# Performance work log

Measured on AMD Instinct MI355X. Metric: run time of the kernel, lower is better.

## Reference

```python
import jax, jax.numpy as jnp
import numpy as np
import math

N_HEADS = 8

def setup_inputs() -> dict:
    key = jax.random.key(0)
    ks = jax.random.split(key, 5)
    B, S, D = 2, 4096, 512
    return {
        "x": jax.random.normal(ks[0], (B, S, D), jnp.float32),
        "W_in": jax.random.normal(ks[1], (D, 3 * D), jnp.float32) * (1.0 / math.sqrt(D)),
        "b_in": jax.random.normal(ks[2], (3 * D,), jnp.float32) * 0.02,
        "W_out": jax.random.normal(ks[3], (D, D), jnp.float32) * (1.0 / math.sqrt(D)),
        "b_out": jax.random.normal(ks[4], (D,), jnp.float32) * 0.02,
        "causal_mask": 1,
    }

def reference(x, W_in, b_in, W_out, b_out, causal_mask):
    B, S, D = x.shape
    H = N_HEADS
    dh = D // H
    qkv = x @ W_in + b_in                      # [B,S,3D]
    q, k, v = jnp.split(qkv, 3, axis=-1)
    # [B,S,D] -> [B,H,S,dh]
    q = q.reshape(B, S, H, dh).transpose(0, 2, 1, 3)
    k = k.reshape(B, S, H, dh).transpose(0, 2, 1, 3)
    v = v.reshape(B, S, H, dh).transpose(0, 2, 1, 3)
    scores = jnp.einsum("bhqd,bhkd->bhqk", q, k)  # [B,H,S,S]
    if causal_mask:
        # strictly upper triangle masked to -inf (before scaling, as in torch code)
        causal = jnp.tril(jnp.ones((S, S), dtype=bool))
        scores = jnp.where(causal, scores, -jnp.inf)
    scores = scores / math.sqrt(dh)
    w = jax.nn.softmax(scores, axis=-1)
    out = jnp.einsum("bhqk,bhkd->bhqd", w, v)     # [B,H,S,dh]
    out = out.transpose(0, 2, 1, 3).reshape(B, S, D)
    return out @ W_out + b_out
```

## Files before the change

kernel.cpp:

```cpp
#include <hip/hip_runtime.h>
#include <stdint.h>

typedef __attribute__((ext_vector_type(8))) short bf16x8;
typedef __attribute__((ext_vector_type(4))) float f32x4;

__device__ __forceinline__ float bf2f(unsigned short b) {
  union { unsigned int u; float f; } c; c.u = ((unsigned int)b) << 16; return c.f;
}
__device__ __forceinline__ unsigned short f2bf(float f) {
  union { float f; unsigned int u; } c; c.f = f;
  unsigned int u = c.u;
  return (unsigned short)((u + 0x7fffu + ((u >> 16) & 1u)) >> 16);
}

__device__ __forceinline__ void gload_lds16(const void* g, void* l) {
  __builtin_amdgcn_global_load_lds((const __attribute__((address_space(1))) void*)g,
                                   (__attribute__((address_space(3))) void*)l,
                                   16, 0, 0);
}

#define QSCALE 0.18033688011112042f


__global__ __launch_bounds__(256) void cvt_x(const float* __restrict__ in,
                                             unsigned short* __restrict__ out, int n4) {
  int i = blockIdx.x * 256 + threadIdx.x;
  if (i < n4) {
    float4 f = ((const float4*)in)[i];
    ushort4 o;
    o.x = f2bf(f.x); o.y = f2bf(f.y); o.z = f2bf(f.z); o.w = f2bf(f.w);
    ((ushort4*)out)[i] = o;
  }
}

__global__ __launch_bounds__(256)
void tw_cvt_t(const float* __restrict__ W, unsigned short* __restrict__ Wt, int N) {
  __shared__ unsigned short T[64][68];
  const int n0 = blockIdx.x * 64, k0 = blockIdx.y * 64;
  const int c = threadIdx.x & 15, r = threadIdx.x >> 4;
#pragma unroll
  for (int i = 0; i < 4; ++i) {
    float4 f = *(const float4*)&W[(size_t)(k0 + i * 16 + r) * N + n0 + c * 4];
    T[c * 4 + 0][i * 16 + r] = f2bf(f.x);
    T[c * 4 + 1][i * 16 + r] = f2bf(f.y);
    T[c * 4 + 2][i * 16 + r] = f2bf(f.z);
    T[c * 4 + 3][i * 16 + r] = f2bf(f.w);
  }
  __syncthreads();
#pragma unroll
  for (int i = 0; i < 4; ++i)
    *(ushort4*)&Wt[(size_t)(n0 + i * 16 + r) * 512 + k0 + c * 4] =
        *(const ushort4*)&T[i * 16 + r][c * 4];
}

__global__ __launch_bounds__(256)
void vtr(const unsigned short* __restrict__ vsd, unsigned short* __restrict__ vt) {
  __shared__ unsigned short T[64][68];
  const int bh = blockIdx.y, s0 = blockIdx.x * 64;
  const int c = threadIdx.x & 15, r = threadIdx.x >> 4;
#pragma unroll
  for (int i = 0; i < 4; ++i) {
    ushort4 u = *(const ushort4*)&vsd[((size_t)bh * 4096 + s0 + i * 16 + r) * 64 + c * 4];
    T[c * 4 + 0][i * 16 + r] = u.x;
    T[c * 4 + 1][i * 16 + r] = u.y;
    T[c * 4 + 2][i * 16 + r] = u.z;
    T[c * 4 + 3][i * 16 + r] = u.w;
  }
  __syncthreads();
#pragma unroll
  for (int i = 0; i < 4; ++i)
    *(ushort4*)&vt[((size_t)bh * 64 + i * 16 + r) * 4096 + s0 + c * 4] =
        *(const ushort4*)&T[i * 16 + r][c * 4];
}


template<int QKV>
__global__ __launch_bounds__(256)
void gemm_bt(const unsigned short* __restrict__ A, const unsigned short* __restrict__ Bt,
             const float* __restrict__ bias, float* __restrict__ Cout,
             unsigned short* __restrict__ qo, unsigned short* __restrict__ ko,
             unsigned short* __restrict__ vo, int M, int N, int K) {
  __shared__ unsigned short As[128 * 64];
  __shared__ unsigned short Bs[128 * 64];
  const int tid = threadIdx.x;
  const int wid = tid >> 6;
  const int lane = tid & 63;
  const int row0 = blockIdx.x * 128;
  const int col0 = blockIdx.y * 128;

  f32x4 acc[4][4];
#pragma unroll
  for (int m = 0; m < 4; ++m)
#pragma unroll
    for (int n = 0; n < 4; ++n)
      acc[m][n] = (f32x4){0.f, 0.f, 0.f, 0.f};

  const int wr = (wid >> 1) * 64;
  const int wc = (wid & 1) * 64;
  const int rw = lane & 15;
  const int nk = K >> 6;

  for (int kt = 0; kt < nk; ++kt) {
    const int k0 = kt << 6;
#pragma unroll
    for (int i = 0; i < 4; ++i) {
      int c = i * 256 + tid;
      int r = c >> 3, kq = (c & 7) << 3;
      gload_lds16(A + (size_t)(row0 + r) * K + k0 + kq, As + (size_t)(i * 256 + wid * 64) * 8);
    }
#pragma unroll
    for (int i = 0; i < 4; ++i) {
      int c = i * 256 + tid;
      int r = c >> 3, kq = (c & 7) << 3;
      gload_lds16(Bt + (size_t)(col0 + r) * K + k0 + kq, Bs + (size_t)(i * 256 + wid * 64) * 8);
    }
    __syncthreads();
#pragma unroll
    for (int ks = 0; ks < 2; ++ks) {
      const int kof = ks * 32 + (lane >> 4) * 8;
      bf16x8 af[4], bfr[4];
#pragma unroll
      for (int m = 0; m < 4; ++m)
        af[m] = *(const bf16x8*)&As[(wr + m * 16 + rw) * 64 + kof];
#pragma unroll
      for (int n = 0; n < 4; ++n)
        bfr[n] = *(const bf16x8*)&Bs[(wc + n * 16 + rw) * 64 + kof];
#pragma unroll
      for (int m = 0; m < 4; ++m)
#pragma unroll
        for (int n = 0; n < 4; ++n)
          acc[m][n] = __builtin_amdgcn_mfma_f32_16x16x32_bf16(af[m], bfr[n], acc[m][n], 0, 0, 0);
    }
    __syncthreads();
  }

  const int lr4 = (lane >> 4) * 4;
  const int lc = lane & 15;
#pragma unroll
  for (int m = 0; m < 4; ++m) {
#pragma unroll
    for (int n = 0; n < 4; ++n) {
      const int col = col0 + wc + n * 16 + lc;
      const float bb = bias[col];
      const int row = row0 + wr + m * 16 + lr4;
      if (QKV) {
        const int which = col >> 9;
        const int rem = col & 511, h = rem >> 6, d = rem & 63;
        const int b = row >> 12, s = row & 4095;
        const float scale = (which == 0) ? QSCALE : 1.0f;
        unsigned short* dst = (which == 0) ? qo : ((which == 1) ? ko : vo);
#pragma unroll
        for (int r2 = 0; r2 < 4; ++r2)
          dst[(((size_t)(b * 8 + h) * 4096 + (s + r2)) << 6) + d] =
              f2bf((acc[m][n][r2] + bb) * scale);
      } else {
#pragma unroll
        for (int r2 = 0; r2 < 4; ++r2)
          Cout[(size_t)(row + r2) * N + col] = acc[m][n][r2] + bb;
      }
    }
  }
}


__global__ __launch_bounds__(256, 3)
void attn_mfma(const unsigned short* __restrict__ Qb, const unsigned short* __restrict__ Kb,
               const unsigned short* __restrict__ Vtb, unsigned short* __restrict__ Ob,
               const int* __restrict__ causal_p) {
  __shared__ unsigned short Ks[2][64 * 64];
  __shared__ unsigned short Vs[2][64 * 64];
  __shared__ unsigned short Ps[4][32 * 64];

  const int tid = threadIdx.x;
  const int wid = tid >> 6;
  const int lane = tid & 63;
  const int lx = lane & 15, ly = lane >> 4, l7 = lane & 7;
  const int p = 31 - blockIdx.x;
  const int bh = blockIdx.y;
  const int causal = *causal_p;
  const int qw = p * 128 + wid * 32;
  const size_t qkbase = (size_t)bh * 4096 * 64;
  const size_t vbase = (size_t)bh * 64 * 4096;

  bf16x8 qf[2][2];
#pragma unroll
  for (int rf = 0; rf < 2; ++rf)
#pragma unroll
    for (int ks = 0; ks < 2; ++ks)
      qf[rf][ks] =
          *(const bf16x8*)(Qb + qkbase + (size_t)(qw + rf * 16 + lx) * 64 + ks * 32 + ly * 8);

  f32x4 o[2][4];
  float mrow[2][4], lpart[2][4];
#pragma unroll
  for (int rf = 0; rf < 2; ++rf) {
#pragma unroll
    for (int df = 0; df < 4; ++df) o[rf][df] = (f32x4){0.f, 0.f, 0.f, 0.f};
#pragma unroll
    for (int r = 0; r < 4; ++r) { mrow[rf][r] = -1e30f; lpart[rf][r] = 0.f; }
  }

  const int ktmax = causal ? (2 * p + 1) : 63;

#pragma unroll
  for (int pass = 0; pass < 2; ++pass) {
    int c = pass * 256 + tid;
    int r = c >> 3, ch = c & 7;
    gload_lds16(Kb + qkbase + (size_t)r * 64 + ((ch ^ (r & 7)) << 3),
                &Ks[0][(size_t)(pass * 256 + wid * 64) * 8]);
    gload_lds16(Vtb + vbase + (size_t)r * 4096 + ((ch ^ (r & 7)) << 3),
                &Vs[0][(size_t)(pass * 256 + wid * 64) * 8]);
  }
  __syncthreads();

  int cur = 0;
  for (int kt = 0; kt <= ktmax; ++kt) {
    if (kt < ktmax) {
      const int nx = kt + 1;
#pragma unroll
      for (int pass = 0; pass < 2; ++pass) {
        int c = pass * 256 + tid;
        int r = c >> 3, ch = c & 7;
        gload_lds16(Kb + qkbase + (size_t)(nx * 64 + r) * 64 + ((ch ^ (r & 7)) << 3),
                    &Ks[cur ^ 1][(size_t)(pass * 256 + wid * 64) * 8]);
        gload_lds16(Vtb + vbase + (size_t)r * 4096 + nx * 64 + ((ch ^ (r & 7)) << 3),
                    &Vs[cur ^ 1][(size_t)(pass * 256 + wid * 64) * 8]);
      }
    }

    const int ktb = kt * 64;
    if (!causal || ktb <= qw + 31) {
      f32x4 s[2][4];
#pragma unroll
      for (int rf = 0; rf < 2; ++rf)
#pragma unroll
        for (int cf = 0; cf < 4; ++cf) s[rf][cf] = (f32x4){0.f, 0.f, 0.f, 0.f};
#pragma unroll
      for (int ks = 0; ks < 2; ++ks) {
        const int kel = ((ks * 4 + ly) ^ l7) << 3;
        bf16x8 kf[4];
#pragma unroll
        for (int cf = 0; cf < 4; ++cf)
          kf[cf] = *(const bf16x8*)&Ks[cur][(cf * 16 + lx) * 64 + kel];
#pragma unroll
        for (int rf = 0; rf < 2; ++rf)
#pragma unroll
          for (int cf = 0; cf < 4; ++cf)
            s[rf][cf] = __builtin_amdgcn_mfma_f32_16x16x32_bf16(qf[rf][ks], kf[cf], s[rf][cf], 0, 0, 0);
      }

      const bool diag = causal && (ktb + 63 > qw);
      float tmx[2][4];
      bool ok = true;
#pragma unroll
      for (int rf = 0; rf < 2; ++rf) {
#pragma unroll
        for (int r = 0; r < 4; ++r) {
          if (diag) {
            const int qg = qw + rf * 16 + ly * 4 + r;
#pragma unroll
            for (int cf = 0; cf < 4; ++cf)
              if (ktb + cf * 16 + lx > qg) s[rf][cf][r] = -1e30f;
          }
          const float a0 = fmaxf(s[rf][0][r], s[rf][1][r]);
          const float a1 = fmaxf(s[rf][2][r], s[rf][3][r]);
          tmx[rf][r] = fmaxf(a0, a1);
          ok = ok && (tmx[rf][r] <= mrow[rf][r] + 8.f);
        }
      }

      if (__all(ok)) {
#pragma unroll
        for (int rf = 0; rf < 2; ++rf) {
#pragma unroll
          for (int r = 0; r < 4; ++r) {
            const float mo = mrow[rf][r];
            const int ql = rf * 16 + ly * 4 + r;
            const int swz = (ql & 7) << 3;
            float lp = 0.f;
#pragma unroll
            for (int cf = 0; cf < 4; ++cf) {
              const float pv = __builtin_amdgcn_exp2f(s[rf][cf][r] - mo);
              lp += pv;
              Ps[wid][ql * 64 + ((cf * 16 + lx) ^ swz)] = f2bf(pv);
            }
            lpart[rf][r] += lp;
          }
        }
      } else {
#pragma unroll
        for (int rf = 0; rf < 2; ++rf) {
#pragma unroll
          for (int r = 0; r < 4; ++r) {
            float tm = tmx[rf][r];
            tm = fmaxf(tm, __shfl_xor(tm, 1));
            tm = fmaxf(tm, __shfl_xor(tm, 2));
            tm = fmaxf(tm, __shfl_xor(tm, 4));
            tm = fmaxf(tm, __shfl_xor(tm, 8));
            const float mo = mrow[rf][r];
            const float mn = fmaxf(mo, tm);
            const float scl = __builtin_amdgcn_exp2f(mo - mn);
            const int ql = rf * 16 + ly * 4 + r;
            const int swz = (ql & 7) << 3;
            float lp = 0.f;
#pragma unroll
            for (int cf = 0; cf < 4; ++cf) {
              const float pv = __builtin_amdgcn_exp2f(s[rf][cf][r] - mn);
              lp += pv;
              Ps[wid][ql * 64 + ((cf * 16 + lx) ^ swz)] = f2bf(pv);
            }
            lpart[rf][r] = lpart[rf][r] * scl + lp;
            mrow[rf][r] = mn;
#pragma unroll
            for (int df = 0; df < 4; ++df) o[rf][df][r] *= scl;
          }
        }
      }

#pragma unroll
      for (int ks = 0; ks < 2; ++ks) {
        const int kel = ((ks * 4 + ly) ^ l7) << 3;
        bf16x8 pa[2], vf[4];
#pragma unroll
        for (int rf = 0; rf < 2; ++rf)
          pa[rf] = *(const bf16x8*)&Ps[wid][(rf * 16 + lx) * 64 + kel];
#pragma unroll
        for (int df = 0; df < 4; ++df)
          vf[df] = *(const bf16x8*)&Vs[cur][(df * 16 + lx) * 64 + kel];
#pragma unroll
        for (int rf = 0; rf < 2; ++rf)
#pragma unroll
          for (int df = 0; df < 4; ++df)
            o[rf][df] = __builtin_amdgcn_mfma_f32_16x16x32_bf16(pa[rf], vf[df], o[rf][df], 0, 0, 0);
      }
    }
    __syncthreads();
    cur ^= 1;
  }

  const int b = bh >> 3, h = bh & 7;
#pragma unroll
  for (int rf = 0; rf < 2; ++rf) {
#pragma unroll
    for (int r = 0; r < 4; ++r) {
      float l = lpart[rf][r];
      l += __shfl_xor(l, 1);
      l += __shfl_xor(l, 2);
      l += __shfl_xor(l, 4);
      l += __shfl_xor(l, 8);
      const float inv = 1.0f / l;
      const int row = b * 4096 + qw + rf * 16 + ly * 4 + r;
#pragma unroll
      for (int df = 0; df < 4; ++df)
        Ob[(size_t)row * 512 + h * 64 + df * 16 + lx] = f2bf(o[rf][df][r] * inv);
    }
  }
}


extern "C" void kernel_launch(void* const* d_in, const int* in_sizes, int n_in,
                              void* d_out, int out_size, void* d_ws, size_t ws_size,
                              hipStream_t stream) {
  const float* x     = (const float*)d_in[0];
  const float* W_in  = (const float*)d_in[1];
  const float* b_in  = (const float*)d_in[2];
  const float* W_out = (const float*)d_in[3];
  const float* b_out = (const float*)d_in[4];
  const int* causal  = (const int*)d_in[5];
  float* out = (float*)d_out;

  unsigned short* xb   = (unsigned short*)d_ws;
  unsigned short* wint = xb + 4194304;
  unsigned short* wout = wint + 786432;
  unsigned short* qb   = wout + 262144;
  unsigned short* kb   = qb + 4194304;
  unsigned short* vt   = kb + 4194304;
  unsigned short* vsd  = (unsigned short*)d_out;

  cvt_x<<<4096, 256, 0, stream>>>(x, xb, 1048576);
  tw_cvt_t<<<dim3(24, 8), 256, 0, stream>>>(W_in, wint, 1536);
  tw_cvt_t<<<dim3(8, 8), 256, 0, stream>>>(W_out, wout, 512);

  gemm_bt<1><<<dim3(64, 12), 256, 0, stream>>>(xb, wint, b_in, nullptr, qb, kb, vsd,
                                               8192, 1536, 512);

  vtr<<<dim3(64, 16), 256, 0, stream>>>(vsd, vt);

  attn_mfma<<<dim3(32, 16), 256, 0, stream>>>(qb, kb, vt, xb, causal);

  gemm_bt<0><<<dim3(64, 4), 256, 0, stream>>>(xb, wout, b_out, out, nullptr, nullptr, nullptr,
                                              8192, 512, 512);
}
```

Measured before the change: 385.2 us.

## Use single-wave attention blocks reading K/V directly from global memory

The attention kernel goes from 4-wave blocks, which shared double-buffered K/V tiles in LDS, to one-wave blocks covering 32 query rows each. Each wave now loads K and V fragments straight from global memory, with no LDS staging and no block barriers. The grid is reordered so that heads vary fastest and the longest causal rows are scheduled first. This removes the syncs and LDS traffic, but K/V reuse across waves is lost, so global/L2 traffic roughly quadruples and there is no prefetch to hide load latency.

```diff
diff --git a/kernel.cpp b/kernel.cpp
--- a/kernel.cpp
+++ b/kernel.cpp
@@ -163,22 +163,18 @@
 }
 
 
-__global__ __launch_bounds__(256, 3)
+__global__ __launch_bounds__(64, 3)
 void attn_mfma(const unsigned short* __restrict__ Qb, const unsigned short* __restrict__ Kb,
                const unsigned short* __restrict__ Vtb, unsigned short* __restrict__ Ob,
                const int* __restrict__ causal_p) {
-  __shared__ unsigned short Ks[2][64 * 64];
-  __shared__ unsigned short Vs[2][64 * 64];
-  __shared__ unsigned short Ps[4][32 * 64];
-
-  const int tid = threadIdx.x;
-  const int wid = tid >> 6;
-  const int lane = tid & 63;
+  __shared__ unsigned short Ps[32 * 64];
+
+  const int lane = threadIdx.x;
   const int lx = lane & 15, ly = lane >> 4, l7 = lane & 7;
-  const int p = 31 - blockIdx.x;
-  const int bh = blockIdx.y;
+  const int bh = blockIdx.x;
+  const int p = 127 - (int)blockIdx.y;
+  const int qw = p * 32;
   const int causal = *causal_p;
-  const int qw = p * 128 + wid * 32;
   const size_t qkbase = (size_t)bh * 4096 * 64;
   const size_t vbase = (size_t)bh * 64 * 4096;
 
@@ -200,142 +196,115 @@
     for (int r = 0; r < 4; ++r) { mrow[rf][r] = -1e30f; lpart[rf][r] = 0.f; }
   }
 
-  const int ktmax = causal ? (2 * p + 1) : 63;
-
-#pragma unroll
-  for (int pass = 0; pass < 2; ++pass) {
-    int c = pass * 256 + tid;
-    int r = c >> 3, ch = c & 7;
-    gload_lds16(Kb + qkbase + (size_t)r * 64 + ((ch ^ (r & 7)) << 3),
-                &Ks[0][(size_t)(pass * 256 + wid * 64) * 8]);
-    gload_lds16(Vtb + vbase + (size_t)r * 4096 + ((ch ^ (r & 7)) << 3),
-                &Vs[0][(size_t)(pass * 256 + wid * 64) * 8]);
-  }
-  __syncthreads();
-
-  int cur = 0;
+  const int ktmax = causal ? ((p * 32 + 31) >> 6) : 63;
+
   for (int kt = 0; kt <= ktmax; ++kt) {
-    if (kt < ktmax) {
-      const int nx = kt + 1;
-#pragma unroll
-      for (int pass = 0; pass < 2; ++pass) {
-        int c = pass * 256 + tid;
-        int r = c >> 3, ch = c & 7;
-        gload_lds16(Kb + qkbase + (size_t)(nx * 64 + r) * 64 + ((ch ^ (r & 7)) << 3),
-                    &Ks[cur ^ 1][(size_t)(pass * 256 + wid * 64) * 8]);
-        gload_lds16(Vtb + vbase + (size_t)r * 4096 + nx * 64 + ((ch ^ (r & 7)) << 3),
-                    &Vs[cur ^ 1][(size_t)(pass * 256 + wid * 64) * 8]);
+    const int ktb = kt * 64;
+
+    f32x4 s[2][4];
+#pragma unroll
+    for (int rf = 0; rf < 2; ++rf)
+#pragma unroll
+      for (int cf = 0; cf < 4; ++cf) s[rf][cf] = (f32x4){0.f, 0.f, 0.f, 0.f};
+#pragma unroll
+    for (int ks = 0; ks < 2; ++ks) {
+      bf16x8 kf[4];
+#pragma unroll
+      for (int cf = 0; cf < 4; ++cf)
+        kf[cf] = *(const bf16x8*)(Kb + qkbase + (size_t)(ktb + cf * 16 + lx) * 64 +
+                                  ks * 32 + ly * 8);
+#pragma unroll
+      for (int rf = 0; rf < 2; ++rf)
+#pragma unroll
+        for (int cf = 0; cf < 4; ++cf)
+          s[rf][cf] = __builtin_amdgcn_mfma_f32_16x16x32_bf16(qf[rf][ks], kf[cf], s[rf][cf], 0, 0, 0);
+    }
+
+    const bool diag = causal && (ktb + 63 > qw);
+    float tmx[2][4];
+    bool ok = true;
+#pragma unroll
+    for (int rf = 0; rf < 2; ++rf) {
+#pragma unroll
+      for (int r = 0; r < 4; ++r) {
+        if (diag) {
+          const int qg = qw + rf * 16 + ly * 4 + r;
+#pragma unroll
+          for (int cf = 0; cf < 4; ++cf)
+            if (ktb + cf * 16 + lx > qg) s[rf][cf][r] = -1e30f;
+        }
+        const float a0 = fmaxf(s[rf][0][r], s[rf][1][r]);
+        const float a1 = fmaxf(s[rf][2][r], s[rf][3][r]);
+        tmx[rf][r] = fmaxf(a0, a1);
+        ok = ok && (tmx[rf][r] <= mrow[rf][r] + 8.f);
       }
     }
 
-    const int ktb = kt * 64;
-    if (!causal || ktb <= qw + 31) {
-      f32x4 s[2][4];
-#pragma unroll
-      for (int rf = 0; rf < 2; ++rf)
-#pragma unroll
-        for (int cf = 0; cf < 4; ++cf) s[rf][cf] = (f32x4){0.f, 0.f, 0.f, 0.f};
-#pragma unroll
-      for (int ks = 0; ks < 2; ++ks) {
-        const int kel = ((ks * 4 + ly) ^ l7) << 3;
-        bf16x8 kf[4];
-#pragma unroll
-        for (int cf = 0; cf < 4; ++cf)
-          kf[cf] = *(const bf16x8*)&Ks[cur][(cf * 16 + lx) * 64 + kel];
-#pragma unroll
-        for (int rf = 0; rf < 2; ++rf)
-#pragma unroll
-          for (int cf = 0; cf < 4; ++cf)
-            s[rf][cf] = __builtin_amdgcn_mfma_f32_16x16x32_bf16(qf[rf][ks], kf[cf], s[rf][cf], 0, 0, 0);
-      }
-
-      const bool diag = causal && (ktb + 63 > qw);
-      float tmx[2][4];
-      bool ok = true;
+    if (__all(ok)) {
 #pragma unroll
       for (int rf = 0; rf < 2; ++rf) {
 #pragma unroll
         for (int r = 0; r < 4; ++r) {
-          if (diag) {
-            const int qg = qw + rf * 16 + ly * 4 + r;
-#pragma unroll
-            for (int cf = 0; cf < 4; ++cf)
-              if (ktb + cf * 16 + lx > qg) s[rf][cf][r] = -1e30f;
+          const float mo = mrow[rf][r];
+          const int ql = rf * 16 + ly * 4 + r;
+          const int swz = (ql & 7) << 3;
+          float lp = 0.f;
+#pragma unroll
+          for (int cf = 0; cf < 4; ++cf) {
+            const float pv = __builtin_amdgcn_exp2f(s[rf][cf][r] - mo);
+            lp += pv;
+            Ps[ql * 64 + ((cf * 16 + lx) ^ swz)] = f2bf(pv);
           }
-          const float a0 = fmaxf(s[rf][0][r], s[rf][1][r]);
-          const float a1 = fmaxf(s[rf][2][r], s[rf][3][r]);
-          tmx[rf][r] = fmaxf(a0, a1);
-          ok = ok && (tmx[rf][r] <= mrow[rf][r] + 8.f);
+          lpart[rf][r] += lp;
         }
       }
-
-      if (__all(ok)) {
-#pragma unroll
-        for (int rf = 0; rf < 2; ++rf) {
-#pragma unroll
-          for (int r = 0; r < 4; ++r) {
-            const float mo = mrow[rf][r];
-            const int ql = rf * 16 + ly * 4 + r;
-            const int swz = (ql & 7) << 3;
-            float lp = 0.f;
-#pragma unroll
-            for (int cf = 0; cf < 4; ++cf) {
-              const float pv = __builtin_amdgcn_exp2f(s[rf][cf][r] - mo);
-              lp += pv;
-              Ps[wid][ql * 64 + ((cf * 16 + lx) ^ swz)] = f2bf(pv);
-            }
-            lpart[rf][r] += lp;
+    } else {
+#pragma unroll
+      for (int rf = 0; rf < 2; ++rf) {
+#pragma unroll
+        for (int r = 0; r < 4; ++r) {
+          float tm = tmx[rf][r];
+          tm = fmaxf(tm, __shfl_xor(tm, 1));
+          tm = fmaxf(tm, __shfl_xor(tm, 2));
+          tm = fmaxf(tm, __shfl_xor(tm, 4));
+          tm = fmaxf(tm, __shfl_xor(tm, 8));
+          const float mo = mrow[rf][r];
+          const float mn = fmaxf(mo, tm);
+          const float scl = __builtin_amdgcn_exp2f(mo - mn);
+          const int ql = rf * 16 + ly * 4 + r;
+          const int swz = (ql & 7) << 3;
+          float lp = 0.f;
+#pragma unroll
+          for (int cf = 0; cf < 4; ++cf) {
+            const float pv = __builtin_amdgcn_exp2f(s[rf][cf][r] - mn);
+            lp += pv;
+            Ps[ql * 64 + ((cf * 16 + lx) ^ swz)] = f2bf(pv);
           }
-        }
-      } else {
-#pragma unroll
-        for (int rf = 0; rf < 2; ++rf) {
-#pragma unroll
-          for (int r = 0; r < 4; ++r) {
-            float tm = tmx[rf][r];
-            tm = fmaxf(tm, __shfl_xor(tm, 1));
-            tm = fmaxf(tm, __shfl_xor(tm, 2));
-            tm = fmaxf(tm, __shfl_xor(tm, 4));
-            tm = fmaxf(tm, __shfl_xor(tm, 8));
-            const float mo = mrow[rf][r];
-            const float mn = fmaxf(mo, tm);
-            const float scl = __builtin_amdgcn_exp2f(mo - mn);
-            const int ql = rf * 16 + ly * 4 + r;
-            const int swz = (ql & 7) << 3;
-            float lp = 0.f;
-#pragma unroll
-            for (int cf = 0; cf < 4; ++cf) {
-              const float pv = __builtin_amdgcn_exp2f(s[rf][cf][r] - mn);
-              lp += pv;
-              Ps[wid][ql * 64 + ((cf * 16 + lx) ^ swz)] = f2bf(pv);
-            }
-            lpart[rf][r] = lpart[rf][r] * scl + lp;
-            mrow[rf][r] = mn;
-#pragma unroll
-            for (int df = 0; df < 4; ++df) o[rf][df][r] *= scl;
-          }
+          lpart[rf][r] = lpart[rf][r] * scl + lp;
+          mrow[rf][r] = mn;
+#pragma unroll
+          for (int df = 0; df < 4; ++df) o[rf][df][r] *= scl;
         }
       }
-
-#pragma unroll
-      for (int ks = 0; ks < 2; ++ks) {
-        const int kel = ((ks * 4 + ly) ^ l7) << 3;
-        bf16x8 pa[2], vf[4];
-#pragma unroll
-        for (int rf = 0; rf < 2; ++rf)
-          pa[rf] = *(const bf16x8*)&Ps[wid][(rf * 16 + lx) * 64 + kel];
+    }
+
+#pragma unroll
+    for (int ks = 0; ks < 2; ++ks) {
+      const int kel = ((ks * 4 + ly) ^ l7) << 3;
+      bf16x8 pa[2], vf[4];
+#pragma unroll
+      for (int rf = 0; rf < 2; ++rf)
+        pa[rf] = *(const bf16x8*)&Ps[(rf * 16 + lx) * 64 + kel];
+#pragma unroll
+      for (int df = 0; df < 4; ++df)
+        vf[df] = *(const bf16x8*)(Vtb + vbase + (size_t)(df * 16 + lx) * 4096 +
+                                  ktb + ks * 32 + ly * 8);
+#pragma unroll
+      for (int rf = 0; rf < 2; ++rf)
 #pragma unroll
         for (int df = 0; df < 4; ++df)
-          vf[df] = *(const bf16x8*)&Vs[cur][(df * 16 + lx) * 64 + kel];
-#pragma unroll
-        for (int rf = 0; rf < 2; ++rf)
-#pragma unroll
-          for (int df = 0; df < 4; ++df)
-            o[rf][df] = __builtin_amdgcn_mfma_f32_16x16x32_bf16(pa[rf], vf[df], o[rf][df], 0, 0, 0);
-      }
-    }
-    __syncthreads();
-    cur ^= 1;
+          o[rf][df] = __builtin_amdgcn_mfma_f32_16x16x32_bf16(pa[rf], vf[df], o[rf][df], 0, 0, 0);
+    }
   }
 
   const int b = bh >> 3, h = bh & 7;
@@ -386,7 +355,7 @@
 
   vtr<<<dim3(64, 16), 256, 0, stream>>>(vsd, vt);
 
-  attn_mfma<<<dim3(32, 16), 256, 0, stream>>>(qb, kb, vt, xb, causal);
+  attn_mfma<<<dim3(16, 128), 64, 0, stream>>>(qb, kb, vt, xb, causal);
 
   gemm_bt<0><<<dim3(64, 4), 256, 0, stream>>>(xb, wout, b_out, out, nullptr, nullptr, nullptr,
                                               8192, 512, 512);
```

After: 387.5 us. No clear change (+0.6%).
